# Performance work log

Measured on AMD Instinct MI355X. Metric: run time of the kernel, lower is better.

Reference implementation:

```python
import jax, jax.numpy as jnp
import numpy as np

E = 1024   # embed_dim
H = 16     # num_heads
D = E // H # head_dim = 64
B = 2
S = 2048

def setup_inputs() -> dict:
    key = jax.random.key(0)
    ks = jax.random.split(key, 11)
    std = 0.02
    return {
        "query": jax.random.normal(ks[0], (B, S, E), jnp.float32),
        "key":   jax.random.normal(ks[1], (B, S, E), jnp.float32),
        "value": jax.random.normal(ks[2], (B, S, E), jnp.float32),
        "Wq": std * jax.random.normal(ks[3], (E, E), jnp.float32),
        "bq": jnp.zeros((E,), jnp.float32),
        "Wk": std * jax.random.normal(ks[4], (D, E), jnp.float32),
        "bk": jnp.zeros((D,), jnp.float32),
        "Wv": std * jax.random.normal(ks[5], (D, E), jnp.float32),
        "bv": jnp.zeros((D,), jnp.float32),
        "Wo": std * jax.random.normal(ks[6], (E, E), jnp.float32),
        "bo": jnp.zeros((E,), jnp.float32),
    }

def reference(query, key, value, Wq, bq, Wk, bk, Wv, bv, Wo, bo):
    b, t, _ = query.shape
    scaling = D ** -0.5
    q = query @ Wq.T + bq                      # [B, T, E]
    k = key @ Wk.T + bk                        # [B, S, D] (single shared KV head)
    v = value @ Wv.T + bv                      # [B, S, D]
    q = q.reshape(b, t, H, D).transpose(0, 2, 1, 3) * scaling  # [B, H, T, D]
    # MQA: broadcast shared k/v across heads inside einsum (no materialized expand)
    attn_weights = jnp.einsum("bhtd,bsd->bhts", q, k)          # [B, H, T, S]
    attn_probs = jax.nn.softmax(attn_weights, axis=-1)
    attn_output = jnp.einsum("bhts,bsd->bhtd", attn_probs, v)  # [B, H, T, D]
    attn_output = attn_output.transpose(0, 2, 1, 3).reshape(b, t, E)
    return attn_output @ Wo.T + bo
```

## Files before the change

### kernel.cpp

```cpp
#include <hip/hip_runtime.h>

#define E_DIM  1024
#define H_HEADS 16
#define D_HEAD  64
#define B_BATCH 2
#define S_SEQ  2048
#define M_ROWS (B_BATCH * S_SEQ)

typedef unsigned short u16;
typedef unsigned int   u32;
typedef __attribute__((ext_vector_type(8))) short bf16x8;
typedef __attribute__((ext_vector_type(4))) short bf16x4;
typedef __attribute__((ext_vector_type(4))) float f32x4;

#define MFMA32(a, b, c) __builtin_amdgcn_mfma_f32_16x16x32_bf16(a, b, c, 0, 0, 0)

#if __has_builtin(__builtin_amdgcn_mfma_f32_16x16x16bf16_1k)
#define HAVE_MFMA16 1
#define MFMA16(a, b, c) __builtin_amdgcn_mfma_f32_16x16x16bf16_1k(a, b, c, 0, 0, 0)
#else
#define HAVE_MFMA16 0
#endif

__device__ __forceinline__ u16 f2bf(float f) {
    union { float f; u32 i; } x; x.f = f;
    u32 r = x.i + 0x7fffu + ((x.i >> 16) & 1u);
    return (u16)(r >> 16);
}

#if __has_builtin(__builtin_amdgcn_cvt_pk_bf16_f32)
typedef __attribute__((ext_vector_type(2))) __bf16 bfp2;
__device__ __forceinline__ u32 pk2(float a, float b) {
    bfp2 t = __builtin_amdgcn_cvt_pk_bf16_f32(a, b);
    union { bfp2 v; u32 u; } c; c.v = t; return c.u;
}
#else
__device__ __forceinline__ u32 pk2(float a, float b) {
    return (u32)f2bf(a) | ((u32)f2bf(b) << 16);
}
#endif

__device__ __forceinline__ bf16x8 cvt8(const float4& a, const float4& b) {
    union { u32 u[4]; bf16x8 v; } t;
    t.u[0] = pk2(a.x, a.y); t.u[1] = pk2(a.z, a.w);
    t.u[2] = pk2(b.x, b.y); t.u[3] = pk2(b.z, b.w);
    return t.v;
}
__device__ __forceinline__ bf16x4 pack4(const f32x4& v) {
    union { u32 u[2]; bf16x4 w; } t;
    t.u[0] = pk2(v[0], v[1]); t.u[1] = pk2(v[2], v[3]);
    return t.w;
}

__device__ __forceinline__ void gl_lds16(const u16* g, u16* l) {
    __builtin_amdgcn_global_load_lds(
        (const __attribute__((address_space(1))) u32*)g,
        (__attribute__((address_space(3))) u32*)l, 16, 0, 0);
}

__global__ __launch_bounds__(256) void kv_proj_kernel(
    const float* __restrict__ key, const float* __restrict__ value,
    const float* __restrict__ Wk, const float* __restrict__ Wv,
    const float* __restrict__ bk, const float* __restrict__ bv,
    u16* __restrict__ Kout, u16* __restrict__ VTout, int M, int K)
{
    const bool vproj = (blockIdx.y == 1);
    const float* A    = vproj ? value : key;
    const float* W    = vproj ? Wv : Wk;
    const float* bias = vproj ? bv : bk;

    __shared__ u16 Asm[64 * 32];
    __shared__ u16 Bsm[64 * 32];

    const int tid = threadIdx.x;
    const int w  = tid >> 6;
    const int ln = tid & 63;
    const int n  = ln & 15;
    const int qd = ln >> 4;
    const int wm = (w & 1) * 32;
    const int wn = (w >> 1) * 32;
    const int m0 = blockIdx.x * 64;

    const int srow = tid >> 2;
    const int scol = (tid & 3) * 8;

    f32x4 acc[2][2];
#pragma unroll
    for (int mt = 0; mt < 2; mt++)
#pragma unroll
        for (int nt = 0; nt < 2; nt++) acc[mt][nt] = (f32x4){0.f, 0.f, 0.f, 0.f};

    for (int k0 = 0; k0 < K; k0 += 32) {
        __syncthreads();
        const float* pa = A + (size_t)(m0 + srow) * K + k0 + scol;
        const float* pw = W + (size_t)srow * K + k0 + scol;
        float4 a0 = ((const float4*)pa)[0], a1 = ((const float4*)pa)[1];
        float4 w0 = ((const float4*)pw)[0], w1 = ((const float4*)pw)[1];
        *(bf16x8*)&Asm[srow * 32 + scol] = cvt8(a0, a1);
        *(bf16x8*)&Bsm[srow * 32 + scol] = cvt8(w0, w1);
        __syncthreads();

        bf16x8 af[2], bfr[2];
#pragma unroll
        for (int t = 0; t < 2; t++) {
            af[t]  = *(const bf16x8*)&Asm[(wm + t * 16 + n) * 32 + qd * 8];
            bfr[t] = *(const bf16x8*)&Bsm[(wn + t * 16 + n) * 32 + qd * 8];
        }
#pragma unroll
        for (int mt = 0; mt < 2; mt++)
#pragma unroll
            for (int nt = 0; nt < 2; nt++)
                acc[mt][nt] = MFMA32(af[mt], bfr[nt], acc[mt][nt]);
    }

    if (!vproj) {
#pragma unroll
        for (int mt = 0; mt < 2; mt++)
#pragma unroll
            for (int r = 0; r < 4; r++) {
                const int row = m0 + wm + mt * 16 + qd * 4 + r;
#pragma unroll
                for (int nt = 0; nt < 2; nt++) {
                    const int col = wn + nt * 16 + n;
                    Kout[(size_t)row * 64 + col] = f2bf(acc[mt][nt][r] + bias[col]);
                }
            }
    } else {
#pragma unroll
        for (int mt = 0; mt < 2; mt++)
#pragma unroll
            for (int nt = 0; nt < 2; nt++) {
                const int col = wn + nt * 16 + n;
                const int row0 = m0 + wm + mt * 16 + qd * 4;
                float b4 = bias[col];
                ushort4 pk;
                pk.x = f2bf(acc[mt][nt][0] + b4);
                pk.y = f2bf(acc[mt][nt][1] + b4);
                pk.z = f2bf(acc[mt][nt][2] + b4);
                pk.w = f2bf(acc[mt][nt][3] + b4);
                *(ushort4*)&VTout[(size_t)col * M + row0] = pk;
            }
    }
}

__global__ __launch_bounds__(256, 2) void ogemm_kernel(
    const u16* __restrict__ A, const float* __restrict__ Wo,
    const float* __restrict__ bias, float* __restrict__ C,
    int M, int N, int K)
{
    __shared__ u16 Asm[2][2][128 * 32];
    __shared__ u16 Bsm[2][2][64 * 32];

    const int tid = threadIdx.x;
    const int w  = tid >> 6;
    const int ln = tid & 63;
    const int n  = ln & 15;
    const int qd = ln >> 4;
    const int ns = (n & 3) ^ (n >> 2);
    const int wm = (w & 1) * 64;
    const int wn = (w >> 1) * 32;

    const int m0 = blockIdx.y * 128;
    const int n0 = blockIdx.x * 64;

    const int srow = tid >> 2;
    const int sblk = tid & 3;
    const int sc   = ((sblk ^ (srow & 3) ^ ((srow >> 2) & 3)) * 8);

    f32x4 acc[4][2];
#pragma unroll
    for (int mt = 0; mt < 4; mt++)
#pragma unroll
        for (int nt = 0; nt < 2; nt++) acc[mt][nt] = (f32x4){0.f, 0.f, 0.f, 0.f};

    float4 wreg[2][2];
    auto stageA = [&](int p, int k0) {
#pragma unroll
        for (int kb = 0; kb < 2; kb++)
#pragma unroll
            for (int g = 0; g < 2; g++) {
                const int row = g * 64 + srow;
                gl_lds16(A + (size_t)(m0 + row) * K + k0 + kb * 32 + sc,
                         &Asm[p][kb][row * 32 + sblk * 8]);
            }
    };
    auto loadW = [&](int k0) {
#pragma unroll
        for (int kb = 0; kb < 2; kb++) {
            const float* pw = Wo + (size_t)(n0 + srow) * K + k0 + kb * 32 + sc;
            wreg[kb][0] = ((const float4*)pw)[0];
            wreg[kb][1] = ((const float4*)pw)[1];
        }
    };
    auto writeW = [&](int p) {
#pragma unroll
        for (int kb = 0; kb < 2; kb++)
            *(bf16x8*)&Bsm[p][kb][srow * 32 + sblk * 8] = cvt8(wreg[kb][0], wreg[kb][1]);
    };
    auto compute = [&](int p) {
        bf16x8 af[4][2], bfr[2][2];
#pragma unroll
        for (int kb = 0; kb < 2; kb++) {
#pragma unroll
            for (int mt = 0; mt < 4; mt++) {
                const int r = wm + mt * 16 + n;
                af[mt][kb] = *(const bf16x8*)&Asm[p][kb][r * 32 + ((qd ^ ns) * 8)];
            }
#pragma unroll
            for (int nt = 0; nt < 2; nt++) {
                const int r = wn + nt * 16 + n;
                bfr[nt][kb] = *(const bf16x8*)&Bsm[p][kb][r * 32 + ((qd ^ ns) * 8)];
            }
        }
#pragma unroll
        for (int kb = 0; kb < 2; kb++)
#pragma unroll
            for (int mt = 0; mt < 4; mt++)
#pragma unroll
                for (int nt = 0; nt < 2; nt++)
                    acc[mt][nt] = MFMA32(af[mt][kb], bfr[nt][kb], acc[mt][nt]);
    };

    stageA(0, 0); loadW(0); writeW(0);

    int p = 0;
    for (int k0 = 64; k0 < K; k0 += 64) {
        __syncthreads();
        stageA(p ^ 1, k0);
        loadW(k0);
        compute(p);
        writeW(p ^ 1);
        p ^= 1;
    }
    __syncthreads();
    compute(p);

    float bb[2];
#pragma unroll
    for (int nt = 0; nt < 2; nt++) bb[nt] = bias[n0 + wn + nt * 16 + n];

#pragma unroll
    for (int mt = 0; mt < 4; mt++)
#pragma unroll
        for (int r = 0; r < 4; r++) {
            const int row = m0 + wm + mt * 16 + qd * 4 + r;
#pragma unroll
            for (int nt = 0; nt < 2; nt++) {
                const int col = n0 + wn + nt * 16 + n;
                C[(size_t)row * N + col] = acc[mt][nt][r] + bb[nt];
            }
        }
}

__global__ __launch_bounds__(256, 2) void mqa_attn_fused_kernel(
    const float* __restrict__ QF, const float* __restrict__ WQ,
    const float* __restrict__ bq,
    const u16* __restrict__ Kt, const u16* __restrict__ VT,
    u16* __restrict__ O, float scaling)
{
    __shared__ u16 lds[32768];
#if !HAVE_MFMA16
    __shared__ u16 psm[4][32 * 128];
#endif

    const int tid = threadIdx.x;
    const int w   = tid >> 6;
    const int ln  = tid & 63;
    const int n   = ln & 15;
    const int qd  = ln >> 4;
    const int lr  = ln >> 2;
    const int blk = ln & 3;
    const int ns  = (n & 3) ^ (n >> 2);
    const int rs  = (lr & 3) ^ (lr >> 2);

    const int bid = blockIdx.x;
    const int qb = bid & 15;
    const int h  = (bid >> 4) & (H_HEADS - 1);
    const int b  = bid >> 8;
    const int q0 = qb * 128;

    const float* ag = QF + (size_t)(b * S_SEQ + q0) * E_DIM;
    const float* wg = WQ + (size_t)(h * 64) * E_DIM;

    const int srow = tid >> 2;
    const int sblk = tid & 3;
    const int sc   = ((sblk ^ (srow & 3) ^ ((srow >> 2) & 3)) * 8);

    float4 areg[2][2][2];
    float4 breg[2][2];
    auto loadP1 = [&](int k0) {
#pragma unroll
        for (int kb = 0; kb < 2; kb++) {
#pragma unroll
            for (int g = 0; g < 2; g++) {
                const float* pa = ag + (size_t)(g * 64 + srow) * E_DIM + k0 + kb * 32 + sc;
                areg[kb][g][0] = ((const float4*)pa)[0];
                areg[kb][g][1] = ((const float4*)pa)[1];
            }
            const float* pw = wg + (size_t)srow * E_DIM + k0 + kb * 32 + sc;
            breg[kb][0] = ((const float4*)pw)[0];
            breg[kb][1] = ((const float4*)pw)[1];
        }
    };
    auto writeP1 = [&](int buf) {
        u16* pa = lds + buf * 12288;
        u16* pb = pa + 8192;
#pragma unroll
        for (int kb = 0; kb < 2; kb++) {
#pragma unroll
            for (int g = 0; g < 2; g++)
                *(bf16x8*)&pa[kb * 4096 + (g * 64 + srow) * 32 + sblk * 8] =
                    cvt8(areg[kb][g][0], areg[kb][g][1]);
            *(bf16x8*)&pb[kb * 2048 + srow * 32 + sblk * 8] =
                cvt8(breg[kb][0], breg[kb][1]);
        }
    };

    float bqv[4];
#pragma unroll
    for (int nt = 0; nt < 4; nt++) bqv[nt] = bq[h * 64 + nt * 16 + n] * scaling;

    f32x4 qacc[2][4];
#pragma unroll
    for (int mt = 0; mt < 2; mt++)
#pragma unroll
        for (int nt = 0; nt < 4; nt++) qacc[mt][nt] = (f32x4){0.f, 0.f, 0.f, 0.f};

    loadP1(0); writeP1(0);
    for (int t = 0; t < 16; ++t) {
        __syncthreads();
        if (t + 1 < 16) loadP1((t + 1) * 64);
        const u16* pa = lds + (t & 1) * 12288;
        const u16* pb = pa + 8192;
        bf16x8 af[2][2], bfr[4][2];
#pragma unroll
        for (int kb = 0; kb < 2; kb++) {
#pragma unroll
            for (int mt = 0; mt < 2; mt++) {
                const int r = w * 32 + mt * 16 + n;
                af[mt][kb] = *(const bf16x8*)&pa[kb * 4096 + r * 32 + ((qd ^ ns) * 8)];
            }
#pragma unroll
            for (int nt = 0; nt < 4; nt++) {
                const int r = nt * 16 + n;
                bfr[nt][kb] = *(const bf16x8*)&pb[kb * 2048 + r * 32 + ((qd ^ ns) * 8)];
            }
        }
#pragma unroll
        for (int kb = 0; kb < 2; kb++)
#pragma unroll
            for (int mt = 0; mt < 2; mt++)
#pragma unroll
                for (int nt = 0; nt < 4; nt++)
                    qacc[mt][nt] = MFMA32(af[mt][kb], bfr[nt][kb], qacc[mt][nt]);
        if (t + 1 < 16) writeP1((t + 1) & 1);
    }

    {
        u16* qsm = lds + 24576;
#pragma unroll
        for (int mt = 0; mt < 2; mt++)
#pragma unroll
            for (int r = 0; r < 4; r++) {
                const int row = w * 32 + mt * 16 + qd * 4 + r;
                const int rsw = (row & 3) ^ ((row >> 2) & 3);
#pragma unroll
                for (int nt = 0; nt < 4; nt++) {
                    const int col = nt * 16 + n;
                    float v = qacc[mt][nt][r] * scaling + bqv[nt];
                    const int kb = col >> 5, c = col & 31;
                    qsm[kb * 4096 + row * 32 + (((c >> 3) ^ rsw) * 8) + (c & 7)] = f2bf(v);
                }
            }
    }
    __syncthreads();

    bf16x8 qa[2][2];
#pragma unroll
    for (int mt = 0; mt < 2; mt++)
#pragma unroll
        for (int kb = 0; kb < 2; kb++) {
            const int row = w * 32 + mt * 16 + n;
            qa[mt][kb] = *(const bf16x8*)&lds[24576 + kb * 4096 + row * 32 + ((qd ^ ns) * 8)];
        }

    const u16* kg = Kt + (size_t)b * S_SEQ * 64;
    const u16* vg = VT + (size_t)b * S_SEQ;

    auto KSM = [&](int p, int kb) -> u16* { return lds + ((p * 2 + kb) * 4096); };
    auto VSM = [&](int p, int c)  -> u16* { return lds + 16384 + ((p * 4 + c) * 2048); };

    auto stageKV = [&](int p, int s0) {
#pragma unroll
        for (int kb = 0; kb < 2; kb++)
#pragma unroll
            for (int j = 0; j < 2; j++) {
                const int row = w * 32 + j * 16 + lr;
                gl_lds16(kg + (size_t)(s0 + row) * 64 + kb * 32 + ((blk ^ rs) * 8),
                         KSM(p, kb) + row * 32 + blk * 8);
            }
#pragma unroll
        for (int j = 0; j < 4; j++) {
            const int d = j * 16 + lr;
            gl_lds16(vg + (size_t)d * M_ROWS + s0 + w * 32 + ((blk ^ rs) * 8),
                     VSM(p, w) + d * 32 + blk * 8);
        }
    };

    stageKV(0, 0);

    f32x4 acc_o[2][4];
    float lsum[2] = {0.f, 0.f};
#pragma unroll
    for (int mt = 0; mt < 2; mt++)
#pragma unroll
        for (int ntd = 0; ntd < 4; ntd++) acc_o[mt][ntd] = (f32x4){0.f, 0.f, 0.f, 0.f};

    int p = 0;
    for (int s0 = 0; s0 < S_SEQ; s0 += 128) {
        __syncthreads();
        if (s0 + 128 < S_SEQ) stageKV(p ^ 1, s0 + 128);

        f32x4 sacc[2][8];
#pragma unroll
        for (int mt = 0; mt < 2; mt++)
#pragma unroll
            for (int nt = 0; nt < 8; nt++) sacc[mt][nt] = (f32x4){0.f, 0.f, 0.f, 0.f};
#pragma unroll
        for (int nt = 0; nt < 8; nt++) {
            const int rowk = nt * 16 + n;
#pragma unroll
            for (int kb = 0; kb < 2; kb++) {
                bf16x8 kf = *(const bf16x8*)&KSM(p, kb)[rowk * 32 + ((qd ^ ns) * 8)];
                sacc[0][nt] = MFMA32(kf, qa[0][kb], sacc[0][nt]);
                sacc[1][nt] = MFMA32(kf, qa[1][kb], sacc[1][nt]);
            }
        }

        bf16x4 pa[2][8];
#pragma unroll
        for (int mt = 0; mt < 2; mt++) {
            float ls = 0.f;
#pragma unroll
            for (int nt = 0; nt < 8; nt++) {
#pragma unroll
                for (int r = 0; r < 4; r++) {
                    float pv = exp2f(sacc[mt][nt][r]);
                    sacc[mt][nt][r] = pv;
                    ls += pv;
                }
                pa[mt][nt] = pack4(sacc[mt][nt]);
            }
            lsum[mt] += ls;
        }

#if HAVE_MFMA16
#pragma unroll
        for (int kk = 0; kk < 8; kk++) {
            const int c = kk >> 1;
            const int lblk = (kk & 1) * 2 + (qd >> 1);
#pragma unroll
            for (int ntd = 0; ntd < 4; ntd++) {
                const int d = ntd * 16 + n;
                bf16x4 bv = *(const bf16x4*)
                    &VSM(p, c)[d * 32 + ((lblk ^ ns) * 8) + (qd & 1) * 4];
                acc_o[0][ntd] = MFMA16(pa[0][kk], bv, acc_o[0][ntd]);
                acc_o[1][ntd] = MFMA16(pa[1][kk], bv, acc_o[1][ntd]);
            }
        }
#else
#pragma unroll
        for (int mt = 0; mt < 2; mt++)
#pragma unroll
            for (int nt = 0; nt < 8; nt++) {
                const int t = mt * 16 + n;
                const int lb = nt * 2 + (qd >> 1);
                union { bf16x4 v; uint2 u; } pw; pw.v = pa[mt][nt];
                *(uint2*)&psm[w][t * 128 + ((lb ^ n) * 8) + (qd & 1) * 4] = pw.u;
            }
        __syncthreads();
#pragma unroll
        for (int kb = 0; kb < 4; kb++) {
            bf16x8 paf[2];
#pragma unroll
            for (int mt = 0; mt < 2; mt++) {
                const int t = mt * 16 + n;
                paf[mt] = *(const bf16x8*)&psm[w][t * 128 + (((kb * 4 + qd) ^ n) * 8)];
            }
#pragma unroll
            for (int ntd = 0; ntd < 4; ntd++) {
                const int d = ntd * 16 + n;
                bf16x8 bv = *(const bf16x8*)&VSM(p, kb)[d * 32 + ((qd ^ ns) * 8)];
                acc_o[0][ntd] = MFMA32(paf[0], bv, acc_o[0][ntd]);
                acc_o[1][ntd] = MFMA32(paf[1], bv, acc_o[1][ntd]);
            }
        }
#endif
        p ^= 1;
    }

#pragma unroll
    for (int mt = 0; mt < 2; mt++) {
        lsum[mt] += __shfl_xor(lsum[mt], 16);
        lsum[mt] += __shfl_xor(lsum[mt], 32);
    }
#pragma unroll
    for (int mt = 0; mt < 2; mt++)
#pragma unroll
        for (int r = 0; r < 4; r++) {
            float inv = 1.f / __shfl(lsum[mt], qd * 4 + r);
            const int grow = b * S_SEQ + q0 + w * 32 + mt * 16 + qd * 4 + r;
#pragma unroll
            for (int ntd = 0; ntd < 4; ntd++) {
                const int gcol = h * D_HEAD + ntd * 16 + n;
                O[(size_t)grow * E_DIM + gcol] = f2bf(acc_o[mt][ntd][r] * inv);
            }
        }
}

extern "C" void kernel_launch(void* const* d_in, const int* in_sizes, int n_in,
                              void* d_out, int out_size, void* d_ws, size_t ws_size,
                              hipStream_t stream) {
    const float* query = (const float*)d_in[0];
    const float* key   = (const float*)d_in[1];
    const float* value = (const float*)d_in[2];
    const float* Wq    = (const float*)d_in[3];
    const float* bq    = (const float*)d_in[4];
    const float* Wk    = (const float*)d_in[5];
    const float* bk    = (const float*)d_in[6];
    const float* Wv    = (const float*)d_in[7];
    const float* bv    = (const float*)d_in[8];
    const float* Wo    = (const float*)d_in[9];
    const float* bo    = (const float*)d_in[10];
    float* out = (float*)d_out;

    const int M = M_ROWS;

    u16* q_bf  = (u16*)d_ws;
    u16* k_bf  = q_bf + (size_t)M * E_DIM;
    u16* vt_bf = k_bf + (size_t)M * D_HEAD;

    dim3 blk(256);
    const float scaling = 0.125f * 1.44269504088896f;

    kv_proj_kernel<<<dim3(M / 64, 2), blk, 0, stream>>>(
        key, value, Wk, Wv, bk, bv, k_bf, vt_bf, M, E_DIM);

    mqa_attn_fused_kernel<<<dim3(512), blk, 0, stream>>>(
        query, Wq, bq, k_bf, vt_bf, q_bf, scaling);

    ogemm_kernel<<<dim3(E_DIM / 64, M / 128), blk, 0, stream>>>(
        q_bf, Wo, bo, out, M, E_DIM, E_DIM);
}
```

Before: 251.9 us.

## Pre-convert query to bf16, stage via direct LDS loads, shrink attention LDS for occupancy

Adds a pass in the prep kernel that converts the fp32 query to bf16 in a scratch buffer (the output buffer), so the fused attention kernel can stage Q tiles with global_load_lds instead of loading fp32 and converting in registers. Attention LDS shrinks by reusing the Q-projection region and single-buffering V with explicit waitcnt/barrier placement, allowing launch bounds of 3 blocks per CU. This trades an extra query read/write pass and tighter V synchronization for halved Q traffic in the attention kernel, fewer registers and higher occupancy.

```diff
diff --git a/kernel.cpp b/kernel.cpp
--- a/kernel.cpp
+++ b/kernel.cpp
@@ -58,28 +58,39 @@
         (__attribute__((address_space(3))) u32*)l, 16, 0, 0);
 }
 
-__global__ __launch_bounds__(256) void kv_proj_kernel(
+__global__ __launch_bounds__(256) void prep_kernel(
+    const float* __restrict__ query, u16* __restrict__ qc,
     const float* __restrict__ key, const float* __restrict__ value,
     const float* __restrict__ Wk, const float* __restrict__ Wv,
     const float* __restrict__ bk, const float* __restrict__ bv,
     u16* __restrict__ Kout, u16* __restrict__ VTout, int M, int K)
 {
-    const bool vproj = (blockIdx.y == 1);
+    __shared__ u16 Asm[64 * 32];
+    __shared__ u16 Bsm[64 * 32];
+
+    const int bid = blockIdx.x;
+    const int tid = threadIdx.x;
+
+    if (bid >= 128) {
+        const size_t i = (size_t)(bid - 128) * 2048 + (size_t)tid * 8;
+        float4 a = ((const float4*)(query + i))[0];
+        float4 b = ((const float4*)(query + i))[1];
+        *(bf16x8*)(qc + i) = cvt8(a, b);
+        return;
+    }
+
+    const bool vproj = (bid >= 64);
     const float* A    = vproj ? value : key;
     const float* W    = vproj ? Wv : Wk;
     const float* bias = vproj ? bv : bk;
 
-    __shared__ u16 Asm[64 * 32];
-    __shared__ u16 Bsm[64 * 32];
-
-    const int tid = threadIdx.x;
     const int w  = tid >> 6;
     const int ln = tid & 63;
     const int n  = ln & 15;
     const int qd = ln >> 4;
     const int wm = (w & 1) * 32;
     const int wn = (w >> 1) * 32;
-    const int m0 = blockIdx.x * 64;
+    const int m0 = (bid & 63) * 64;
 
     const int srow = tid >> 2;
     const int scol = (tid & 3) * 8;
@@ -252,13 +263,13 @@
         }
 }
 
-__global__ __launch_bounds__(256, 2) void mqa_attn_fused_kernel(
-    const float* __restrict__ QF, const float* __restrict__ WQ,
+__global__ __launch_bounds__(256, 3) void mqa_attn_fused_kernel(
+    const u16* __restrict__ QC, const float* __restrict__ WQ,
     const float* __restrict__ bq,
     const u16* __restrict__ Kt, const u16* __restrict__ VT,
     u16* __restrict__ O, float scaling)
 {
-    __shared__ u16 lds[32768];
+    __shared__ u16 lds[24576];
 #if !HAVE_MFMA16
     __shared__ u16 psm[4][32 * 128];
 #endif
@@ -279,41 +290,38 @@
     const int b  = bid >> 8;
     const int q0 = qb * 128;
 
-    const float* ag = QF + (size_t)(b * S_SEQ + q0) * E_DIM;
+    const u16*   ag = QC + (size_t)(b * S_SEQ + q0) * E_DIM;
     const float* wg = WQ + (size_t)(h * 64) * E_DIM;
 
     const int srow = tid >> 2;
     const int sblk = tid & 3;
     const int sc   = ((sblk ^ (srow & 3) ^ ((srow >> 2) & 3)) * 8);
 
-    float4 areg[2][2][2];
     float4 breg[2][2];
-    auto loadP1 = [&](int k0) {
+    auto stageA1 = [&](int buf, int k0) {
+        u16* pa = lds + buf * 12288;
+#pragma unroll
+        for (int kb = 0; kb < 2; kb++)
+#pragma unroll
+            for (int g = 0; g < 2; g++) {
+                const int row = g * 64 + srow;
+                gl_lds16(ag + (size_t)row * E_DIM + k0 + kb * 32 + sc,
+                         pa + kb * 4096 + row * 32 + sblk * 8);
+            }
+    };
+    auto loadB1 = [&](int k0) {
 #pragma unroll
         for (int kb = 0; kb < 2; kb++) {
-#pragma unroll
-            for (int g = 0; g < 2; g++) {
-                const float* pa = ag + (size_t)(g * 64 + srow) * E_DIM + k0 + kb * 32 + sc;
-                areg[kb][g][0] = ((const float4*)pa)[0];
-                areg[kb][g][1] = ((const float4*)pa)[1];
-            }
             const float* pw = wg + (size_t)srow * E_DIM + k0 + kb * 32 + sc;
             breg[kb][0] = ((const float4*)pw)[0];
             breg[kb][1] = ((const float4*)pw)[1];
         }
     };
-    auto writeP1 = [&](int buf) {
-        u16* pa = lds + buf * 12288;
-        u16* pb = pa + 8192;
-#pragma unroll
-        for (int kb = 0; kb < 2; kb++) {
-#pragma unroll
-            for (int g = 0; g < 2; g++)
-                *(bf16x8*)&pa[kb * 4096 + (g * 64 + srow) * 32 + sblk * 8] =
-                    cvt8(areg[kb][g][0], areg[kb][g][1]);
-            *(bf16x8*)&pb[kb * 2048 + srow * 32 + sblk * 8] =
-                cvt8(breg[kb][0], breg[kb][1]);
-        }
+    auto writeB1 = [&](int buf) {
+        u16* pb = lds + buf * 12288 + 8192;
+#pragma unroll
+        for (int kb = 0; kb < 2; kb++)
+            *(bf16x8*)&pb[kb * 2048 + srow * 32 + sblk * 8] = cvt8(breg[kb][0], breg[kb][1]);
     };
 
     float bqv[4];
@@ -326,10 +334,10 @@
 #pragma unroll
         for (int nt = 0; nt < 4; nt++) qacc[mt][nt] = (f32x4){0.f, 0.f, 0.f, 0.f};
 
-    loadP1(0); writeP1(0);
+    stageA1(0, 0); loadB1(0); writeB1(0);
     for (int t = 0; t < 16; ++t) {
         __syncthreads();
-        if (t + 1 < 16) loadP1((t + 1) * 64);
+        if (t + 1 < 16) { stageA1((t + 1) & 1, (t + 1) * 64); loadB1((t + 1) * 64); }
         const u16* pa = lds + (t & 1) * 12288;
         const u16* pb = pa + 8192;
         bf16x8 af[2][2], bfr[4][2];
@@ -353,11 +361,11 @@
 #pragma unroll
                 for (int nt = 0; nt < 4; nt++)
                     qacc[mt][nt] = MFMA32(af[mt][kb], bfr[nt][kb], qacc[mt][nt]);
-        if (t + 1 < 16) writeP1((t + 1) & 1);
+        if (t + 1 < 16) writeB1((t + 1) & 1);
     }
 
     {
-        u16* qsm = lds + 24576;
+        u16* qsm = lds;
 #pragma unroll
         for (int mt = 0; mt < 2; mt++)
 #pragma unroll
@@ -381,16 +389,17 @@
 #pragma unroll
         for (int kb = 0; kb < 2; kb++) {
             const int row = w * 32 + mt * 16 + n;
-            qa[mt][kb] = *(const bf16x8*)&lds[24576 + kb * 4096 + row * 32 + ((qd ^ ns) * 8)];
-        }
+            qa[mt][kb] = *(const bf16x8*)&lds[kb * 4096 + row * 32 + ((qd ^ ns) * 8)];
+        }
+    __syncthreads();
 
     const u16* kg = Kt + (size_t)b * S_SEQ * 64;
     const u16* vg = VT + (size_t)b * S_SEQ;
 
     auto KSM = [&](int p, int kb) -> u16* { return lds + ((p * 2 + kb) * 4096); };
-    auto VSM = [&](int p, int c)  -> u16* { return lds + 16384 + ((p * 4 + c) * 2048); };
-
-    auto stageKV = [&](int p, int s0) {
+    auto VSM = [&](int c)  -> u16* { return lds + 16384 + (c * 2048); };
+
+    auto stageK = [&](int p, int s0) {
 #pragma unroll
         for (int kb = 0; kb < 2; kb++)
 #pragma unroll
@@ -399,15 +408,15 @@
                 gl_lds16(kg + (size_t)(s0 + row) * 64 + kb * 32 + ((blk ^ rs) * 8),
                          KSM(p, kb) + row * 32 + blk * 8);
             }
+    };
+    auto stageV = [&](int s0) {
 #pragma unroll
         for (int j = 0; j < 4; j++) {
             const int d = j * 16 + lr;
             gl_lds16(vg + (size_t)d * M_ROWS + s0 + w * 32 + ((blk ^ rs) * 8),
-                     VSM(p, w) + d * 32 + blk * 8);
-        }
-    };
-
-    stageKV(0, 0);
+                     VSM(w) + d * 32 + blk * 8);
+        }
+    };
 
     f32x4 acc_o[2][4];
     float lsum[2] = {0.f, 0.f};
@@ -416,10 +425,15 @@
 #pragma unroll
         for (int ntd = 0; ntd < 4; ntd++) acc_o[mt][ntd] = (f32x4){0.f, 0.f, 0.f, 0.f};
 
+    stageK(0, 0); stageV(0);
+    asm volatile("s_waitcnt vmcnt(4)" ::: "memory");
+    __builtin_amdgcn_s_barrier();
+    __builtin_amdgcn_sched_barrier(0);
+
     int p = 0;
     for (int s0 = 0; s0 < S_SEQ; s0 += 128) {
-        __syncthreads();
-        if (s0 + 128 < S_SEQ) stageKV(p ^ 1, s0 + 128);
+        const bool more = (s0 + 128 < S_SEQ);
+        if (more) stageK(p ^ 1, s0 + 128);
 
         f32x4 sacc[2][8];
 #pragma unroll
@@ -454,6 +468,11 @@
             lsum[mt] += ls;
         }
 
+        if (more) asm volatile("s_waitcnt vmcnt(4)" ::: "memory");
+        else      asm volatile("s_waitcnt vmcnt(0)" ::: "memory");
+        __builtin_amdgcn_s_barrier();
+        __builtin_amdgcn_sched_barrier(0);
+
 #if HAVE_MFMA16
 #pragma unroll
         for (int kk = 0; kk < 8; kk++) {
@@ -463,7 +482,7 @@
             for (int ntd = 0; ntd < 4; ntd++) {
                 const int d = ntd * 16 + n;
                 bf16x4 bv = *(const bf16x4*)
-                    &VSM(p, c)[d * 32 + ((lblk ^ ns) * 8) + (qd & 1) * 4];
+                    &VSM(c)[d * 32 + ((lblk ^ ns) * 8) + (qd & 1) * 4];
                 acc_o[0][ntd] = MFMA16(pa[0][kk], bv, acc_o[0][ntd]);
                 acc_o[1][ntd] = MFMA16(pa[1][kk], bv, acc_o[1][ntd]);
             }
@@ -490,12 +509,19 @@
 #pragma unroll
             for (int ntd = 0; ntd < 4; ntd++) {
                 const int d = ntd * 16 + n;
-                bf16x8 bv = *(const bf16x8*)&VSM(p, kb)[d * 32 + ((qd ^ ns) * 8)];
+                bf16x8 bv = *(const bf16x8*)&VSM(kb)[d * 32 + ((qd ^ ns) * 8)];
                 acc_o[0][ntd] = MFMA32(paf[0], bv, acc_o[0][ntd]);
                 acc_o[1][ntd] = MFMA32(paf[1], bv, acc_o[1][ntd]);
             }
         }
 #endif
+
+        if (more) {
+            asm volatile("s_waitcnt vmcnt(0)" ::: "memory");
+            __builtin_amdgcn_s_barrier();
+            __builtin_amdgcn_sched_barrier(0);
+            stageV(s0 + 128);
+        }
         p ^= 1;
     }
 
@@ -540,14 +566,16 @@
     u16* k_bf  = q_bf + (size_t)M * E_DIM;
     u16* vt_bf = k_bf + (size_t)M * D_HEAD;
 
+    u16* qc_bf = (u16*)d_out;
+
     dim3 blk(256);
     const float scaling = 0.125f * 1.44269504088896f;
 
-    kv_proj_kernel<<<dim3(M / 64, 2), blk, 0, stream>>>(
-        key, value, Wk, Wv, bk, bv, k_bf, vt_bf, M, E_DIM);
+    prep_kernel<<<dim3(2176), blk, 0, stream>>>(
+        query, qc_bf, key, value, Wk, Wv, bk, bv, k_bf, vt_bf, M, E_DIM);
 
     mqa_attn_fused_kernel<<<dim3(512), blk, 0, stream>>>(
-        query, Wq, bq, k_bf, vt_bf, q_bf, scaling);
+        qc_bf, Wq, bq, k_bf, vt_bf, q_bf, scaling);
 
     ogemm_kernel<<<dim3(E_DIM / 64, M / 128), blk, 0, stream>>>(
         q_bf, Wo, bo, out, M, E_DIM, E_DIM);
```

Result: no change. 247.7 us (-1.7%).

## Pre-convert query and Wq to bf16 and stage Q-proj tiles via direct global-to-LDS loads

Applied to the files above, without the earlier changes.

The KV projection kernel becomes a prep kernel whose extra blocks also convert query and Wq from fp32 to bf16 into scratch buffers, using the output buffer for the converted query. The fused attention kernel then stages its Q-projection tiles with global_load_lds 16-byte copies instead of fp32 register loads followed by conversion and LDS stores. The aim is to halve the fp32 reads done inside the attention kernel, where query rows are re-read once per head, and to free the registers and instructions used for staging. In exchange there is an extra pass over query that writes bf16 to memory, plus a reliance on d_out being large enough and not in use until the final GEMM.

```diff
diff --git a/kernel.cpp b/kernel.cpp
--- a/kernel.cpp
+++ b/kernel.cpp
@@ -58,28 +58,44 @@
         (__attribute__((address_space(3))) u32*)l, 16, 0, 0);
 }
 
-__global__ __launch_bounds__(256) void kv_proj_kernel(
+__global__ __launch_bounds__(256) void prep_kernel(
+    const float* __restrict__ query, u16* __restrict__ qc,
+    const float* __restrict__ Wq, u16* __restrict__ wq_bf,
     const float* __restrict__ key, const float* __restrict__ value,
     const float* __restrict__ Wk, const float* __restrict__ Wv,
     const float* __restrict__ bk, const float* __restrict__ bv,
     u16* __restrict__ Kout, u16* __restrict__ VTout, int M, int K)
 {
-    const bool vproj = (blockIdx.y == 1);
+    __shared__ u16 Asm[64 * 32];
+    __shared__ u16 Bsm[64 * 32];
+
+    const int bid = blockIdx.x;
+    const int tid = threadIdx.x;
+
+    if (bid >= 128) {
+        const int cbid = bid - 128;
+        const float* src; u16* dst; size_t base;
+        if (cbid < 2048) { src = query; dst = qc;    base = (size_t)cbid * 2048; }
+        else             { src = Wq;    dst = wq_bf; base = (size_t)(cbid - 2048) * 2048; }
+        const size_t i = base + (size_t)tid * 8;
+        float4 a = ((const float4*)(src + i))[0];
+        float4 b = ((const float4*)(src + i))[1];
+        *(bf16x8*)(dst + i) = cvt8(a, b);
+        return;
+    }
+
+    const bool vproj = (bid >= 64);
     const float* A    = vproj ? value : key;
     const float* W    = vproj ? Wv : Wk;
     const float* bias = vproj ? bv : bk;
 
-    __shared__ u16 Asm[64 * 32];
-    __shared__ u16 Bsm[64 * 32];
-
-    const int tid = threadIdx.x;
     const int w  = tid >> 6;
     const int ln = tid & 63;
     const int n  = ln & 15;
     const int qd = ln >> 4;
     const int wm = (w & 1) * 32;
     const int wn = (w >> 1) * 32;
-    const int m0 = blockIdx.x * 64;
+    const int m0 = (bid & 63) * 64;
 
     const int srow = tid >> 2;
     const int scol = (tid & 3) * 8;
@@ -253,7 +269,7 @@
 }
 
 __global__ __launch_bounds__(256, 2) void mqa_attn_fused_kernel(
-    const float* __restrict__ QF, const float* __restrict__ WQ,
+    const u16* __restrict__ QC, const u16* __restrict__ WQ,
     const float* __restrict__ bq,
     const u16* __restrict__ Kt, const u16* __restrict__ VT,
     u16* __restrict__ O, float scaling)
@@ -279,41 +295,28 @@
     const int b  = bid >> 8;
     const int q0 = qb * 128;
 
-    const float* ag = QF + (size_t)(b * S_SEQ + q0) * E_DIM;
-    const float* wg = WQ + (size_t)(h * 64) * E_DIM;
+    const u16* ag = QC + (size_t)(b * S_SEQ + q0) * E_DIM;
+    const u16* wg = WQ + (size_t)(h * 64) * E_DIM;
 
     const int srow = tid >> 2;
     const int sblk = tid & 3;
     const int sc   = ((sblk ^ (srow & 3) ^ ((srow >> 2) & 3)) * 8);
 
-    float4 areg[2][2][2];
-    float4 breg[2][2];
-    auto loadP1 = [&](int k0) {
-#pragma unroll
-        for (int kb = 0; kb < 2; kb++) {
-#pragma unroll
-            for (int g = 0; g < 2; g++) {
-                const float* pa = ag + (size_t)(g * 64 + srow) * E_DIM + k0 + kb * 32 + sc;
-                areg[kb][g][0] = ((const float4*)pa)[0];
-                areg[kb][g][1] = ((const float4*)pa)[1];
-            }
-            const float* pw = wg + (size_t)srow * E_DIM + k0 + kb * 32 + sc;
-            breg[kb][0] = ((const float4*)pw)[0];
-            breg[kb][1] = ((const float4*)pw)[1];
-        }
-    };
-    auto writeP1 = [&](int buf) {
+    auto stageP1 = [&](int buf, int k0) {
         u16* pa = lds + buf * 12288;
         u16* pb = pa + 8192;
 #pragma unroll
-        for (int kb = 0; kb < 2; kb++) {
-#pragma unroll
-            for (int g = 0; g < 2; g++)
-                *(bf16x8*)&pa[kb * 4096 + (g * 64 + srow) * 32 + sblk * 8] =
-                    cvt8(areg[kb][g][0], areg[kb][g][1]);
-            *(bf16x8*)&pb[kb * 2048 + srow * 32 + sblk * 8] =
-                cvt8(breg[kb][0], breg[kb][1]);
-        }
+        for (int kb = 0; kb < 2; kb++)
+#pragma unroll
+            for (int g = 0; g < 2; g++) {
+                const int row = g * 64 + srow;
+                gl_lds16(ag + (size_t)row * E_DIM + k0 + kb * 32 + sc,
+                         pa + kb * 4096 + row * 32 + sblk * 8);
+            }
+#pragma unroll
+        for (int kb = 0; kb < 2; kb++)
+            gl_lds16(wg + (size_t)srow * E_DIM + k0 + kb * 32 + sc,
+                     pb + kb * 2048 + srow * 32 + sblk * 8);
     };
 
     float bqv[4];
@@ -326,10 +329,10 @@
 #pragma unroll
         for (int nt = 0; nt < 4; nt++) qacc[mt][nt] = (f32x4){0.f, 0.f, 0.f, 0.f};
 
-    loadP1(0); writeP1(0);
+    stageP1(0, 0);
     for (int t = 0; t < 16; ++t) {
         __syncthreads();
-        if (t + 1 < 16) loadP1((t + 1) * 64);
+        if (t + 1 < 16) stageP1((t + 1) & 1, (t + 1) * 64);
         const u16* pa = lds + (t & 1) * 12288;
         const u16* pb = pa + 8192;
         bf16x8 af[2][2], bfr[4][2];
@@ -353,7 +356,6 @@
 #pragma unroll
                 for (int nt = 0; nt < 4; nt++)
                     qacc[mt][nt] = MFMA32(af[mt][kb], bfr[nt][kb], qacc[mt][nt]);
-        if (t + 1 < 16) writeP1((t + 1) & 1);
     }
 
     {
@@ -539,15 +541,18 @@
     u16* q_bf  = (u16*)d_ws;
     u16* k_bf  = q_bf + (size_t)M * E_DIM;
     u16* vt_bf = k_bf + (size_t)M * D_HEAD;
+    u16* wq_bf = vt_bf + (size_t)M * D_HEAD;
+
+    u16* qc_bf = (u16*)d_out;
 
     dim3 blk(256);
     const float scaling = 0.125f * 1.44269504088896f;
 
-    kv_proj_kernel<<<dim3(M / 64, 2), blk, 0, stream>>>(
-        key, value, Wk, Wv, bk, bv, k_bf, vt_bf, M, E_DIM);
+    prep_kernel<<<dim3(2688), blk, 0, stream>>>(
+        query, qc_bf, Wq, wq_bf, key, value, Wk, Wv, bk, bv, k_bf, vt_bf, M, E_DIM);
 
     mqa_attn_fused_kernel<<<dim3(512), blk, 0, stream>>>(
-        query, Wq, bq, k_bf, vt_bf, q_bf, scaling);
+        qc_bf, wq_bf, bq, k_bf, vt_bf, q_bf, scaling);
 
     ogemm_kernel<<<dim3(E_DIM / 64, M / 128), blk, 0, stream>>>(
         q_bf, Wo, bo, out, M, E_DIM, E_DIM);
```

Result: faster. 237.9 us (-5.6%).
